# Kernel optimization log

Hardware: AMD Instinct MI355X
Metric: run time of the kernel (lower is better)

The kernel has to match this reference:

```python
import jax, jax.numpy as jnp
import numpy as np

IN, OUT, R = 512, 512, 4
H = (IN + OUT) * R + OUT  # 4608, LSTM hidden size


def setup_inputs() -> dict:
    key = jax.random.key(0)
    ks = jax.random.split(key, 8)
    B = 256
    x = jax.random.normal(ks[0], (B, IN), dtype=jnp.float32)
    h0 = jax.random.normal(ks[1], (B, H), dtype=jnp.float32)
    c0 = jax.random.normal(ks[2], (B, H), dtype=jnp.float32)
    s_ih = 1.0 / np.sqrt(H)
    W_ih = jax.random.uniform(ks[3], (4 * H, IN), dtype=jnp.float32, minval=-s_ih, maxval=s_ih)
    W_hh = jax.random.uniform(ks[4], (4 * H, H), dtype=jnp.float32, minval=-s_ih, maxval=s_ih)
    b_ih = jax.random.uniform(ks[5], (4 * H,), dtype=jnp.float32, minval=-s_ih, maxval=s_ih)
    b_hh = jax.random.uniform(ks[6], (4 * H,), dtype=jnp.float32, minval=-s_ih, maxval=s_ih)
    initial_weight = jax.random.normal(ks[7], (1, OUT, IN), dtype=jnp.float32)
    initial_bias = jnp.zeros((1, OUT), dtype=jnp.float32)
    return {"x": x, "h0": h0, "c0": c0, "W_ih": W_ih, "W_hh": W_hh,
            "b_ih": b_ih, "b_hh": b_hh,
            "initial_weight": initial_weight, "initial_bias": initial_bias}


def reference(x, h0, c0, W_ih, W_hh, b_ih, b_hh, initial_weight, initial_bias):
    B = x.shape[0]
    # Batched LSTMCell (the per-sample python loop in the original is
    # mathematically identical to one batched cell).  PyTorch gate order: i,f,g,o.
    gates = x @ W_ih.T + b_ih + h0 @ W_hh.T + b_hh  # [B, 4H]
    i, f, g, o = jnp.split(gates, 4, axis=-1)
    c_new = jax.nn.sigmoid(f) * c0 + jax.nn.sigmoid(i) * jnp.tanh(g)
    h_new = jax.nn.sigmoid(o) * jnp.tanh(c_new)  # [B, H]
    # Low-rank per-sample weight deltas
    dw1 = h_new[:, : OUT * R].reshape(B, OUT, R)
    dw2 = h_new[:, OUT * R: OUT * R + IN * R].reshape(B, R, IN)
    db = h_new[:, OUT * R + IN * R:]  # [B, OUT]
    weight = initial_weight + jnp.einsum('bor,bri->boi', dw1, dw2)  # [B, OUT, IN]
    bias = initial_bias + db  # [B, OUT]
    y = jnp.einsum('bi,boi->bo', x, weight) + bias
    return (y, h_new, c_new)
```

## Files before the change

### kernel.cpp

```cpp
#include <hip/hip_runtime.h>

#define B_DIM 256
#define H_DIM 4608
#define K_X   512
#define K_TOT 5120
#define NSTEP 160

typedef __attribute__((ext_vector_type(8))) short  short8;
typedef __attribute__((ext_vector_type(4))) float  floatx4;

#define BAR() do { \
  __builtin_amdgcn_sched_barrier(0); \
  asm volatile("s_waitcnt lgkmcnt(0)" ::: "memory"); \
  __builtin_amdgcn_s_barrier(); \
  __builtin_amdgcn_sched_barrier(0); \
} while (0)

static __device__ __forceinline__ unsigned pkbf(float a, float b){
  unsigned ua = (__float_as_uint(a) + 0x8000u) >> 16;
  unsigned ub = (__float_as_uint(b) + 0x8000u) & 0xFFFF0000u;
  return ua | ub;
}
static __device__ __forceinline__ float sigm(float v){ return 1.0f / (1.0f + __expf(-v)); }
static __device__ __forceinline__ float tanh_fast(float v){
  float ax = fabsf(v);
  float e  = __expf(-2.0f * ax);
  float t  = (1.0f - e) / (1.0f + e);
  return copysignf(t, v);
}

__global__ __launch_bounds__(256) void conv_kernel(
    const float* __restrict__ x, const float* __restrict__ h0,
    unsigned short* __restrict__ Abf, float* __restrict__ z)
{
  const int t = threadIdx.x;
  if (blockIdx.x == 0) ((float4*)z)[t] = make_float4(0.f, 0.f, 0.f, 0.f);
  const long e = ((long)blockIdx.x * 256 + t) * 8;
  const int  b = (int)(e / K_TOT);
  const int  k = (int)(e - (long)b * K_TOT);
  const float* src = (k < K_X) ? (x + (long)b * K_X + k)
                               : (h0 + (long)b * H_DIM + (k - K_X));
  float4 v0 = *(const float4*)src;
  float4 v1 = *(const float4*)(src + 4);
  uint4 wv;
  wv.x = pkbf(v0.x, v0.y); wv.y = pkbf(v0.z, v0.w);
  wv.z = pkbf(v1.x, v1.y); wv.w = pkbf(v1.z, v1.w);
  *(uint4*)(Abf + e) = wv;
}

__global__ __launch_bounds__(256, 2) void lstm_gates_kernel(
    const unsigned short* __restrict__ Abf,
    const float* __restrict__ x,
    const float* __restrict__ c0,
    const float* __restrict__ Wih, const float* __restrict__ Whh,
    const float* __restrict__ bih, const float* __restrict__ bhh,
    float* __restrict__ outH, float* __restrict__ outC,
    float* __restrict__ z)
{
  __shared__ __align__(16) unsigned short Bs[2][64 * 32];

  const int t    = threadIdx.x;
  const int j0   = blockIdx.x * 16;
  const int w    = t >> 6;
  const int l    = t & 63;
  const int q    = l >> 4;
  const int col  = l & 15;
  const int jj   = j0 + col;
  const int wrow = w * 64;

  const long aBase = (long)(wrow + col) * K_TOT + q * 8;

  const int  rB   = t >> 2;
  const int  cB   = t & 3;
  const int  gate = rB >> 4;
  const int  jl   = rB & 15;
  const long wrowg = (long)gate * H_DIM + j0 + jl;
  const float* __restrict__ pWx = Wih + wrowg * K_X   + cB * 8;
  const float* __restrict__ pWh = Whh + wrowg * H_DIM + cB * 8;

  char* ldsBase = (char*)&Bs[0][0];
  const int bwByte = rB  * 64 + ((cB ^ ((rB  >> 1) & 3)) << 4);
  const int brByte = col * 64 + ((q  ^ ((col >> 1) & 3)) << 4);

  floatx4 acc[4][4];
  #pragma unroll
  for (int nt = 0; nt < 4; ++nt){
    float bsum = bih[nt * H_DIM + jj] + bhh[nt * H_DIM + jj];
    floatx4 v = {bsum, bsum, bsum, bsum};
    #pragma unroll
    for (int mt = 0; mt < 4; ++mt) acc[mt][nt] = v;
  }

  float4 pb[4][2];
  short8 af0[4], af1[4];

  auto issueB = [&](int kt, int slot){
    const int ko = kt * 32;
    const float* p = (ko < K_X) ? (pWx + ko) : (pWh + (ko - K_X));
    pb[slot][0] = *(const float4*)p;
    pb[slot][1] = *(const float4*)(p + 4);
  };
  auto writeB = [&](int slot, int buf){
    uint4 wv;
    wv.x = pkbf(pb[slot][0].x, pb[slot][0].y);
    wv.y = pkbf(pb[slot][0].z, pb[slot][0].w);
    wv.z = pkbf(pb[slot][1].x, pb[slot][1].y);
    wv.w = pkbf(pb[slot][1].z, pb[slot][1].w);
    *(uint4*)(ldsBase + buf * 4096 + bwByte) = wv;
  };
  auto loadA = [&](int kt, short8* af){
    const unsigned short* p = Abf + (aBase + kt * 32);
    #pragma unroll
    for (int mt = 0; mt < 4; ++mt)
      af[mt] = *(const short8*)(p + (long)mt * (16 * K_TOT));
  };
  auto mfmaStep = [&](int buf, const short8* af){
    short8 bf[4];
    #pragma unroll
    for (int nt = 0; nt < 4; ++nt)
      bf[nt] = *(const short8*)(ldsBase + buf * 4096 + brByte + nt * 1024);
    #pragma unroll
    for (int mt = 0; mt < 4; ++mt)
      #pragma unroll
      for (int nt = 0; nt < 4; ++nt)
        acc[mt][nt] = __builtin_amdgcn_mfma_f32_16x16x32_bf16(af[mt], bf[nt], acc[mt][nt], 0, 0, 0);
  };

  issueB(0, 0); issueB(1, 1); issueB(2, 2); issueB(3, 3);
  loadA(0, af0);
  writeB(0, 0);
  BAR();

  #pragma unroll 1
  for (int k = 0; k < NSTEP; k += 4){
    loadA(k + 1, af1);
    if (k + 4 < NSTEP) issueB(k + 4, 0);
    mfmaStep(0, af0);
    writeB(1, 1);
    BAR();
    loadA(k + 2, af0);
    if (k + 5 < NSTEP) issueB(k + 5, 1);
    mfmaStep(1, af1);
    writeB(2, 0);
    BAR();
    loadA(k + 3, af1);
    if (k + 6 < NSTEP) issueB(k + 6, 2);
    mfmaStep(0, af0);
    writeB(3, 1);
    BAR();
    if (k + 4 < NSTEP) loadA(k + 4, af0);
    if (k + 7 < NSTEP) issueB(k + 7, 3);
    mfmaStep(1, af1);
    if (k + 4 < NSTEP) writeB(0, 0);
    BAR();
  }

  const bool isDw2 = (j0 >= 2048) && (j0 < 4096);
  const int  rIdx  = (j0 - 2048) >> 9;
  const int  i0    = (j0 - 2048) & 511;

  #pragma unroll
  for (int mt = 0; mt < 4; ++mt){
    #pragma unroll
    for (int r2 = 0; r2 < 4; ++r2){
      const int brow = wrow + mt * 16 + q * 4 + r2;
      float iv = acc[mt][0][r2];
      float fv = acc[mt][1][r2];
      float gv = acc[mt][2][r2];
      float ov = acc[mt][3][r2];
      float cp = c0[(long)brow * H_DIM + jj];
      float cn = sigm(fv) * cp + sigm(iv) * tanh_fast(gv);
      float hn = sigm(ov) * tanh_fast(cn);
      outH[(long)brow * H_DIM + jj] = hn;
      outC[(long)brow * H_DIM + jj] = cn;
      if (isDw2){
        float v = hn * x[(long)brow * K_X + i0 + col];
        v += __shfl_xor(v, 1); v += __shfl_xor(v, 2);
        v += __shfl_xor(v, 4); v += __shfl_xor(v, 8);
        if (col == 0) atomicAdd(&z[brow * 4 + rIdx], v);
      }
    }
  }
}

__global__ __launch_bounds__(256) void y_kernel(
    const unsigned short* __restrict__ Abf,
    const float* __restrict__ hnew,
    const float* __restrict__ W0, const float* __restrict__ b0,
    const float* __restrict__ z,
    float* __restrict__ y)
{
  __shared__ __align__(16) unsigned short Ws[16 * 512];
  const int t    = threadIdx.x;
  const int w    = t >> 6;
  const int l    = t & 63;
  const int q    = l >> 4;
  const int col  = l & 15;
  const int n0   = blockIdx.x * 16;
  const int wrow = w * 64;

  {
    const int r  = t >> 4;
    const int kc = (t & 15) * 32;
    const float* src = W0 + (long)(n0 + r) * 512 + kc;
    #pragma unroll
    for (int j = 0; j < 4; ++j){
      float4 a = *(const float4*)(src + j * 8);
      float4 b = *(const float4*)(src + j * 8 + 4);
      uint4 wv;
      wv.x = pkbf(a.x, a.y); wv.y = pkbf(a.z, a.w);
      wv.z = pkbf(b.x, b.y); wv.w = pkbf(b.z, b.w);
      const int cch = (kc >> 3) + j;
      const int sw  = cch ^ (r & 7);
      *(uint4*)((char*)Ws + r * 1024 + sw * 16) = wv;
    }
  }
  __syncthreads();

  const long aBase = (long)(wrow + col) * K_TOT + q * 8;
  floatx4 acc[4];
  #pragma unroll
  for (int mt = 0; mt < 4; ++mt) acc[mt] = (floatx4){0.f, 0.f, 0.f, 0.f};

  #pragma unroll 4
  for (int ks = 0; ks < 16; ++ks){
    const int sw = (ks * 4 + q) ^ (col & 7);
    short8 bf = *(const short8*)((char*)Ws + col * 1024 + sw * 16);
    #pragma unroll
    for (int mt = 0; mt < 4; ++mt){
      short8 af = *(const short8*)(Abf + aBase + ks * 32 + (long)mt * (16 * K_TOT));
      acc[mt] = __builtin_amdgcn_mfma_f32_16x16x32_bf16(af, bf, acc[mt], 0, 0, 0);
    }
  }

  const int   o  = n0 + col;
  const float bo = b0[o];
  #pragma unroll
  for (int mt = 0; mt < 4; ++mt){
    #pragma unroll
    for (int r2 = 0; r2 < 4; ++r2){
      const int brow = wrow + mt * 16 + q * 4 + r2;
      const float* hr = hnew + (long)brow * H_DIM;
      float4 d1 = *(const float4*)(hr + o * 4);
      float4 zr = *(const float4*)(z + brow * 4);
      float val = acc[mt][r2] + bo + hr[4096 + o]
                + d1.x * zr.x + d1.y * zr.y + d1.z * zr.z + d1.w * zr.w;
      y[(long)brow * 512 + o] = val;
    }
  }
}

extern "C" void kernel_launch(void* const* d_in, const int* in_sizes, int n_in,
                              void* d_out, int out_size, void* d_ws, size_t ws_size,
                              hipStream_t stream)
{
  (void)in_sizes; (void)n_in; (void)out_size; (void)ws_size;
  const float* x   = (const float*)d_in[0];
  const float* h0  = (const float*)d_in[1];
  const float* c0  = (const float*)d_in[2];
  const float* Wih = (const float*)d_in[3];
  const float* Whh = (const float*)d_in[4];
  const float* bih = (const float*)d_in[5];
  const float* bhh = (const float*)d_in[6];
  const float* W0  = (const float*)d_in[7];
  const float* b0  = (const float*)d_in[8];

  float* out  = (float*)d_out;
  float* y    = out;
  float* outH = out + 131072;
  float* outC = out + 131072 + 1179648;

  unsigned short* Abf = (unsigned short*)d_ws;
  float* z = (float*)((char*)d_ws + (size_t)B_DIM * K_TOT * 2);

  hipLaunchKernelGGL(conv_kernel, dim3(640), dim3(256), 0, stream, x, h0, Abf, z);
  hipLaunchKernelGGL(lstm_gates_kernel, dim3(288), dim3(256), 0, stream,
                     Abf, x, c0, Wih, Whh, bih, bhh, outH, outC, z);
  hipLaunchKernelGGL(y_kernel, dim3(32), dim3(256), 0, stream, Abf, outH, W0, b0, z, y);
}
```

Baseline: 677.5 us.

## Split-K the LSTM gate GEMM with atomic accumulation and a separate cell kernel

The gate GEMM is split four ways along K, so 1152 blocks run instead of 288, and the occupancy hint rises to 4 blocks per CU. This addresses the under-filled GPU: 288 blocks is barely more than one wave of blocks across the CUs. Partial sums go by float atomicAdd into a zeroed fp32 gate buffer, and a new cell_kernel then adds biases, applies the LSTM nonlinearity and computes the dw2 dot products. The cost is an extra kernel launch, zeroing and re-reading about 19 MB of gate scratch, and a large number of global atomics.

Result: slower. 860.4 us (+27.0%).

```diff
diff --git a/kernel.cpp b/kernel.cpp
--- a/kernel.cpp
+++ b/kernel.cpp
@@ -4,7 +4,10 @@
 #define H_DIM 4608
 #define K_X   512
 #define K_TOT 5120
-#define NSTEP 160
+#define NSPLIT 4
+#define KSPL  (K_TOT / NSPLIT)
+#define NSTEP (KSPL / 32)
+#define G_STRIDE 18432
 
 typedef __attribute__((ext_vector_type(8))) short  short8;
 typedef __attribute__((ext_vector_type(4))) float  floatx4;
@@ -31,10 +34,18 @@
 
 __global__ __launch_bounds__(256) void conv_kernel(
     const float* __restrict__ x, const float* __restrict__ h0,
-    unsigned short* __restrict__ Abf, float* __restrict__ z)
+    unsigned short* __restrict__ Abf, float* __restrict__ G,
+    float* __restrict__ z)
 {
   const int t = threadIdx.x;
   if (blockIdx.x == 0) ((float4*)z)[t] = make_float4(0.f, 0.f, 0.f, 0.f);
+
+  {
+    float4 z4 = make_float4(0.f, 0.f, 0.f, 0.f);
+    for (int i = blockIdx.x * 256 + t; i < 1179648; i += 640 * 256)
+      ((float4*)G)[i] = z4;
+  }
+
   const long e = ((long)blockIdx.x * 256 + t) * 8;
   const int  b = (int)(e / K_TOT);
   const int  k = (int)(e - (long)b * K_TOT);
@@ -48,27 +59,26 @@
   *(uint4*)(Abf + e) = wv;
 }
 
-__global__ __launch_bounds__(256, 2) void lstm_gates_kernel(
+__global__ __launch_bounds__(256, 4) void lstm_gates_kernel(
     const unsigned short* __restrict__ Abf,
-    const float* __restrict__ x,
-    const float* __restrict__ c0,
     const float* __restrict__ Wih, const float* __restrict__ Whh,
-    const float* __restrict__ bih, const float* __restrict__ bhh,
-    float* __restrict__ outH, float* __restrict__ outC,
-    float* __restrict__ z)
+    float* __restrict__ G)
 {
   __shared__ __align__(16) unsigned short Bs[2][64 * 32];
 
-  const int t    = threadIdx.x;
-  const int j0   = blockIdx.x * 16;
-  const int w    = t >> 6;
-  const int l    = t & 63;
-  const int q    = l >> 4;
-  const int col  = l & 15;
-  const int jj   = j0 + col;
-  const int wrow = w * 64;
-
-  const long aBase = (long)(wrow + col) * K_TOT + q * 8;
+  const int t     = threadIdx.x;
+  const int tile  = blockIdx.x >> 2;
+  const int split = blockIdx.x & 3;
+  const int kbase = split * KSPL;
+  const int j0    = tile * 16;
+  const int w     = t >> 6;
+  const int l     = t & 63;
+  const int q     = l >> 4;
+  const int col   = l & 15;
+  const int jj    = j0 + col;
+  const int wrow  = w * 64;
+
+  const long aBase = (long)(wrow + col) * K_TOT + kbase + q * 8;
 
   const int  rB   = t >> 2;
   const int  cB   = t & 3;
@@ -84,18 +94,16 @@
 
   floatx4 acc[4][4];
   #pragma unroll
-  for (int nt = 0; nt < 4; ++nt){
-    float bsum = bih[nt * H_DIM + jj] + bhh[nt * H_DIM + jj];
-    floatx4 v = {bsum, bsum, bsum, bsum};
-    #pragma unroll
-    for (int mt = 0; mt < 4; ++mt) acc[mt][nt] = v;
-  }
+  for (int mt = 0; mt < 4; ++mt)
+    #pragma unroll
+    for (int nt = 0; nt < 4; ++nt)
+      acc[mt][nt] = (floatx4){0.f, 0.f, 0.f, 0.f};
 
   float4 pb[4][2];
   short8 af0[4], af1[4];
 
   auto issueB = [&](int kt, int slot){
-    const int ko = kt * 32;
+    const int ko = kbase + kt * 32;
     const float* p = (ko < K_X) ? (pWx + ko) : (pWh + (ko - K_X));
     pb[slot][0] = *(const float4*)p;
     pb[slot][1] = *(const float4*)(p + 4);
@@ -155,30 +163,67 @@
     BAR();
   }
 
-  const bool isDw2 = (j0 >= 2048) && (j0 < 4096);
-  const int  rIdx  = (j0 - 2048) >> 9;
-  const int  i0    = (j0 - 2048) & 511;
-
   #pragma unroll
   for (int mt = 0; mt < 4; ++mt){
     #pragma unroll
     for (int r2 = 0; r2 < 4; ++r2){
       const int brow = wrow + mt * 16 + q * 4 + r2;
-      float iv = acc[mt][0][r2];
-      float fv = acc[mt][1][r2];
-      float gv = acc[mt][2][r2];
-      float ov = acc[mt][3][r2];
-      float cp = c0[(long)brow * H_DIM + jj];
-      float cn = sigm(fv) * cp + sigm(iv) * tanh_fast(gv);
-      float hn = sigm(ov) * tanh_fast(cn);
-      outH[(long)brow * H_DIM + jj] = hn;
-      outC[(long)brow * H_DIM + jj] = cn;
-      if (isDw2){
-        float v = hn * x[(long)brow * K_X + i0 + col];
-        v += __shfl_xor(v, 1); v += __shfl_xor(v, 2);
-        v += __shfl_xor(v, 4); v += __shfl_xor(v, 8);
-        if (col == 0) atomicAdd(&z[brow * 4 + rIdx], v);
-      }
+      float* gp = G + (long)brow * G_STRIDE + jj;
+      atomicAdd(gp,            acc[mt][0][r2]);
+      atomicAdd(gp + H_DIM,    acc[mt][1][r2]);
+      atomicAdd(gp + 2*H_DIM,  acc[mt][2][r2]);
+      atomicAdd(gp + 3*H_DIM,  acc[mt][3][r2]);
+    }
+  }
+}
+
+__global__ __launch_bounds__(256) void cell_kernel(
+    const float* __restrict__ G, const float* __restrict__ c0,
+    const float* __restrict__ bih, const float* __restrict__ bhh,
+    const float* __restrict__ x,
+    float* __restrict__ outH, float* __restrict__ outC, float* __restrict__ z)
+{
+  const int b = blockIdx.x;
+  const int t = threadIdx.x;
+  const int l = t & 63;
+
+  const float4* Gf  = (const float4*)(G  + (long)b * G_STRIDE);
+  const float4* cf  = (const float4*)(c0 + (long)b * H_DIM);
+  const float4* bi4 = (const float4*)bih;
+  const float4* bh4 = (const float4*)bhh;
+  const float4* x4  = (const float4*)(x + (long)b * K_X);
+  float4* H4 = (float4*)(outH + (long)b * H_DIM);
+  float4* C4 = (float4*)(outC + (long)b * H_DIM);
+
+  for (int v = t; v < 1152; v += 256){
+    float4 gi = Gf[v];
+    float4 gf = Gf[1152 + v];
+    float4 gg = Gf[2304 + v];
+    float4 go = Gf[3456 + v];
+    float4 b0i = bi4[v],        b0h = bh4[v];
+    float4 b1i = bi4[1152 + v], b1h = bh4[1152 + v];
+    float4 b2i = bi4[2304 + v], b2h = bh4[2304 + v];
+    float4 b3i = bi4[3456 + v], b3h = bh4[3456 + v];
+    gi.x += b0i.x + b0h.x; gi.y += b0i.y + b0h.y; gi.z += b0i.z + b0h.z; gi.w += b0i.w + b0h.w;
+    gf.x += b1i.x + b1h.x; gf.y += b1i.y + b1h.y; gf.z += b1i.z + b1h.z; gf.w += b1i.w + b1h.w;
+    gg.x += b2i.x + b2h.x; gg.y += b2i.y + b2h.y; gg.z += b2i.z + b2h.z; gg.w += b2i.w + b2h.w;
+    go.x += b3i.x + b3h.x; go.y += b3i.y + b3h.y; go.z += b3i.z + b3h.z; go.w += b3i.w + b3h.w;
+    float4 cp = cf[v];
+    float4 cn, hn;
+    cn.x = sigm(gf.x) * cp.x + sigm(gi.x) * tanh_fast(gg.x); hn.x = sigm(go.x) * tanh_fast(cn.x);
+    cn.y = sigm(gf.y) * cp.y + sigm(gi.y) * tanh_fast(gg.y); hn.y = sigm(go.y) * tanh_fast(cn.y);
+    cn.z = sigm(gf.z) * cp.z + sigm(gi.z) * tanh_fast(gg.z); hn.z = sigm(go.z) * tanh_fast(cn.z);
+    cn.w = sigm(gf.w) * cp.w + sigm(gi.w) * tanh_fast(gg.w); hn.w = sigm(go.w) * tanh_fast(cn.w);
+    C4[v] = cn;
+    H4[v] = hn;
+    const int j = v * 4;
+    if (j >= 2048 && j < 4096){
+      const int r = (j - 2048) >> 9;
+      float4 xv = x4[v - 512 - (r << 7)];
+      float s = hn.x * xv.x + hn.y * xv.y + hn.z * xv.z + hn.w * xv.w;
+      s += __shfl_xor(s, 32); s += __shfl_xor(s, 16); s += __shfl_xor(s, 8);
+      s += __shfl_xor(s, 4);  s += __shfl_xor(s, 2);  s += __shfl_xor(s, 1);
+      if (l == 0) atomicAdd(&z[b * 4 + r], s);
     }
   }
 }
@@ -272,9 +317,12 @@
 
   unsigned short* Abf = (unsigned short*)d_ws;
   float* z = (float*)((char*)d_ws + (size_t)B_DIM * K_TOT * 2);
-
-  hipLaunchKernelGGL(conv_kernel, dim3(640), dim3(256), 0, stream, x, h0, Abf, z);
-  hipLaunchKernelGGL(lstm_gates_kernel, dim3(288), dim3(256), 0, stream,
-                     Abf, x, c0, Wih, Whh, bih, bhh, outH, outC, z);
+  float* G = (float*)((char*)d_ws + (size_t)B_DIM * K_TOT * 2 + 4096);
+
+  hipLaunchKernelGGL(conv_kernel, dim3(640), dim3(256), 0, stream, x, h0, Abf, G, z);
+  hipLaunchKernelGGL(lstm_gates_kernel, dim3(288 * NSPLIT), dim3(256), 0, stream,
+                     Abf, Wih, Whh, G);
+  hipLaunchKernelGGL(cell_kernel, dim3(256), dim3(256), 0, stream,
+                     G, c0, bih, bhh, x, outH, outC, z);
   hipLaunchKernelGGL(y_kernel, dim3(32), dim3(256), 0, stream, Abf, outH, W0, b0, z, y);
 }
```

## Split fused LSTM GEMM into transposed LDS-free GEMM plus separate cell kernel

Applied to the files above, without the earlier changes.

Replaces the fused gates GEMM and cell kernel with two kernels. The first computes the transposed gate matrix, with weights as the A operand loaded straight from global memory and converted to bf16 in registers, over 1152 blocks with no LDS or barriers. The second applies the cell nonlinearity through LDS-staged tiles and writes coalesced h/c. This raises parallelism and removes barrier stalls, at the cost of a 19 MB fp32 gate intermediate round-trip through memory and an extra launch.

After: 986.4 us. 45.6% more time.

```diff
diff --git a/kernel.cpp b/kernel.cpp
--- a/kernel.cpp
+++ b/kernel.cpp
@@ -4,17 +4,10 @@
 #define H_DIM 4608
 #define K_X   512
 #define K_TOT 5120
-#define NSTEP 160
-
-typedef __attribute__((ext_vector_type(8))) short  short8;
-typedef __attribute__((ext_vector_type(4))) float  floatx4;
-
-#define BAR() do { \
-  __builtin_amdgcn_sched_barrier(0); \
-  asm volatile("s_waitcnt lgkmcnt(0)" ::: "memory"); \
-  __builtin_amdgcn_s_barrier(); \
-  __builtin_amdgcn_sched_barrier(0); \
-} while (0)
+
+typedef __attribute__((ext_vector_type(8))) short    short8;
+typedef __attribute__((ext_vector_type(4))) float    floatx4;
+typedef __attribute__((ext_vector_type(4))) unsigned uintx4;
 
 static __device__ __forceinline__ unsigned pkbf(float a, float b){
   unsigned ua = (__float_as_uint(a) + 0x8000u) >> 16;
@@ -35,6 +28,7 @@
 {
   const int t = threadIdx.x;
   if (blockIdx.x == 0) ((float4*)z)[t] = make_float4(0.f, 0.f, 0.f, 0.f);
+
   const long e = ((long)blockIdx.x * 256 + t) * 8;
   const int  b = (int)(e / K_TOT);
   const int  k = (int)(e - (long)b * K_TOT);
@@ -48,137 +42,117 @@
   *(uint4*)(Abf + e) = wv;
 }
 
-__global__ __launch_bounds__(256, 2) void lstm_gates_kernel(
+__global__ __launch_bounds__(256, 4) void gatesT_kernel(
     const unsigned short* __restrict__ Abf,
+    const float* __restrict__ Wih, const float* __restrict__ Whh,
+    float* __restrict__ GT)
+{
+  const int t   = threadIdx.x;
+  const int w   = t >> 6;
+  const int l   = t & 63;
+  const int q   = l >> 4;
+  const int col = l & 15;
+  const int m0  = blockIdx.x * 16;
+  const int wb  = w * 64;
+
+  const float* __restrict__ pWx = Wih + (long)(m0 + col) * K_X   + q * 8;
+  const float* __restrict__ pWh = Whh + (long)(m0 + col) * H_DIM + q * 8;
+  const unsigned short* __restrict__ pA0 = Abf + (long)(wb + col) * K_TOT + q * 8;
+  const unsigned short* __restrict__ pA1 = pA0 + (long)16 * K_TOT;
+  const unsigned short* __restrict__ pA2 = pA0 + (long)32 * K_TOT;
+  const unsigned short* __restrict__ pA3 = pA0 + (long)48 * K_TOT;
+
+  floatx4 acc0 = {0.f,0.f,0.f,0.f}, acc1 = acc0, acc2 = acc0, acc3 = acc0;
+
+#define GSTEP(PW, AOFF) do {                                                   \
+    floatx4 w0 = *(const floatx4*)(PW);                                        \
+    floatx4 w1 = *(const floatx4*)((PW) + 4);                                  \
+    union { uintx4 u; short8 s; } cv;                                          \
+    cv.u = (uintx4){ pkbf(w0.x,w0.y), pkbf(w0.z,w0.w),                         \
+                     pkbf(w1.x,w1.y), pkbf(w1.z,w1.w) };                       \
+    short8 af = cv.s;                                                          \
+    acc0 = __builtin_amdgcn_mfma_f32_16x16x32_bf16(af, *(const short8*)(pA0 + (AOFF)), acc0, 0, 0, 0); \
+    acc1 = __builtin_amdgcn_mfma_f32_16x16x32_bf16(af, *(const short8*)(pA1 + (AOFF)), acc1, 0, 0, 0); \
+    acc2 = __builtin_amdgcn_mfma_f32_16x16x32_bf16(af, *(const short8*)(pA2 + (AOFF)), acc2, 0, 0, 0); \
+    acc3 = __builtin_amdgcn_mfma_f32_16x16x32_bf16(af, *(const short8*)(pA3 + (AOFF)), acc3, 0, 0, 0); \
+  } while (0)
+
+  #pragma unroll 4
+  for (int kt = 0; kt < 16; ++kt)
+    GSTEP(pWx + kt * 32, kt * 32);
+  #pragma unroll 4
+  for (int kt = 0; kt < 144; ++kt)
+    GSTEP(pWh + kt * 32, K_X + kt * 32);
+#undef GSTEP
+
+  float* __restrict__ gp = GT + (long)(m0 + q * 4) * B_DIM + wb + col;
+  #pragma unroll
+  for (int r = 0; r < 4; ++r){
+    gp[(long)r * B_DIM +  0] = acc0[r];
+    gp[(long)r * B_DIM + 16] = acc1[r];
+    gp[(long)r * B_DIM + 32] = acc2[r];
+    gp[(long)r * B_DIM + 48] = acc3[r];
+  }
+}
+
+__global__ __launch_bounds__(256) void cell_kernel(
+    const float* __restrict__ GT, const float* __restrict__ c0,
+    const float* __restrict__ bih, const float* __restrict__ bhh,
     const float* __restrict__ x,
-    const float* __restrict__ c0,
-    const float* __restrict__ Wih, const float* __restrict__ Whh,
-    const float* __restrict__ bih, const float* __restrict__ bhh,
-    float* __restrict__ outH, float* __restrict__ outC,
-    float* __restrict__ z)
-{
-  __shared__ __align__(16) unsigned short Bs[2][64 * 32];
-
-  const int t    = threadIdx.x;
-  const int j0   = blockIdx.x * 16;
-  const int w    = t >> 6;
-  const int l    = t & 63;
-  const int q    = l >> 4;
-  const int col  = l & 15;
-  const int jj   = j0 + col;
-  const int wrow = w * 64;
-
-  const long aBase = (long)(wrow + col) * K_TOT + q * 8;
-
-  const int  rB   = t >> 2;
-  const int  cB   = t & 3;
-  const int  gate = rB >> 4;
-  const int  jl   = rB & 15;
-  const long wrowg = (long)gate * H_DIM + j0 + jl;
-  const float* __restrict__ pWx = Wih + wrowg * K_X   + cB * 8;
-  const float* __restrict__ pWh = Whh + wrowg * H_DIM + cB * 8;
-
-  char* ldsBase = (char*)&Bs[0][0];
-  const int bwByte = rB  * 64 + ((cB ^ ((rB  >> 1) & 3)) << 4);
-  const int brByte = col * 64 + ((q  ^ ((col >> 1) & 3)) << 4);
-
-  floatx4 acc[4][4];
-  #pragma unroll
-  for (int nt = 0; nt < 4; ++nt){
-    float bsum = bih[nt * H_DIM + jj] + bhh[nt * H_DIM + jj];
-    floatx4 v = {bsum, bsum, bsum, bsum};
-    #pragma unroll
-    for (int mt = 0; mt < 4; ++mt) acc[mt][nt] = v;
-  }
-
-  float4 pb[4][2];
-  short8 af0[4], af1[4];
-
-  auto issueB = [&](int kt, int slot){
-    const int ko = kt * 32;
-    const float* p = (ko < K_X) ? (pWx + ko) : (pWh + (ko - K_X));
-    pb[slot][0] = *(const float4*)p;
-    pb[slot][1] = *(const float4*)(p + 4);
-  };
-  auto writeB = [&](int slot, int buf){
-    uint4 wv;
-    wv.x = pkbf(pb[slot][0].x, pb[slot][0].y);
-    wv.y = pkbf(pb[slot][0].z, pb[slot][0].w);
-    wv.z = pkbf(pb[slot][1].x, pb[slot][1].y);
-    wv.w = pkbf(pb[slot][1].z, pb[slot][1].w);
-    *(uint4*)(ldsBase + buf * 4096 + bwByte) = wv;
-  };
-  auto loadA = [&](int kt, short8* af){
-    const unsigned short* p = Abf + (aBase + kt * 32);
-    #pragma unroll
-    for (int mt = 0; mt < 4; ++mt)
-      af[mt] = *(const short8*)(p + (long)mt * (16 * K_TOT));
-  };
-  auto mfmaStep = [&](int buf, const short8* af){
-    short8 bf[4];
-    #pragma unroll
-    for (int nt = 0; nt < 4; ++nt)
-      bf[nt] = *(const short8*)(ldsBase + buf * 4096 + brByte + nt * 1024);
-    #pragma unroll
-    for (int mt = 0; mt < 4; ++mt)
-      #pragma unroll
-      for (int nt = 0; nt < 4; ++nt)
-        acc[mt][nt] = __builtin_amdgcn_mfma_f32_16x16x32_bf16(af[mt], bf[nt], acc[mt][nt], 0, 0, 0);
-  };
-
-  issueB(0, 0); issueB(1, 1); issueB(2, 2); issueB(3, 3);
-  loadA(0, af0);
-  writeB(0, 0);
-  BAR();
-
-  #pragma unroll 1
-  for (int k = 0; k < NSTEP; k += 4){
-    loadA(k + 1, af1);
-    if (k + 4 < NSTEP) issueB(k + 4, 0);
-    mfmaStep(0, af0);
-    writeB(1, 1);
-    BAR();
-    loadA(k + 2, af0);
-    if (k + 5 < NSTEP) issueB(k + 5, 1);
-    mfmaStep(1, af1);
-    writeB(2, 0);
-    BAR();
-    loadA(k + 3, af1);
-    if (k + 6 < NSTEP) issueB(k + 6, 2);
-    mfmaStep(0, af0);
-    writeB(3, 1);
-    BAR();
-    if (k + 4 < NSTEP) loadA(k + 4, af0);
-    if (k + 7 < NSTEP) issueB(k + 7, 3);
-    mfmaStep(1, af1);
-    if (k + 4 < NSTEP) writeB(0, 0);
-    BAR();
-  }
-
+    float* __restrict__ outH, float* __restrict__ outC, float* __restrict__ z)
+{
+  __shared__ float cs[128][67];
+  __shared__ float hs[128][67];
+  __shared__ float xs[128][67];
+
+  const int t  = threadIdx.x;
+  const int j0 = (blockIdx.x >> 1) * 64;
+  const int bh = blockIdx.x & 1;
   const bool isDw2 = (j0 >= 2048) && (j0 < 4096);
-  const int  rIdx  = (j0 - 2048) >> 9;
-  const int  i0    = (j0 - 2048) & 511;
-
-  #pragma unroll
-  for (int mt = 0; mt < 4; ++mt){
-    #pragma unroll
-    for (int r2 = 0; r2 < 4; ++r2){
-      const int brow = wrow + mt * 16 + q * 4 + r2;
-      float iv = acc[mt][0][r2];
-      float fv = acc[mt][1][r2];
-      float gv = acc[mt][2][r2];
-      float ov = acc[mt][3][r2];
-      float cp = c0[(long)brow * H_DIM + jj];
-      float cn = sigm(fv) * cp + sigm(iv) * tanh_fast(gv);
-      float hn = sigm(ov) * tanh_fast(cn);
-      outH[(long)brow * H_DIM + jj] = hn;
-      outC[(long)brow * H_DIM + jj] = cn;
-      if (isDw2){
-        float v = hn * x[(long)brow * K_X + i0 + col];
-        v += __shfl_xor(v, 1); v += __shfl_xor(v, 2);
-        v += __shfl_xor(v, 4); v += __shfl_xor(v, 8);
-        if (col == 0) atomicAdd(&z[brow * 4 + rIdx], v);
-      }
+  const int rIdx = (j0 - 2048) >> 9;
+  const int i0   = (j0 - 2048) & 511;
+
+  {
+    const int jj = t & 63;
+    const int bb = t >> 6;
+    for (int p = 0; p < 32; ++p){
+      const int b = p * 4 + bb;
+      cs[b][jj] = c0[(long)(bh * 128 + b) * H_DIM + j0 + jj];
+      if (isDw2) xs[b][jj] = x[(long)(bh * 128 + b) * K_X + i0 + jj];
+    }
+  }
+  __syncthreads();
+
+  {
+    const int b  = t & 127;
+    const int jh = t >> 7;
+    float zacc = 0.f;
+    for (int jj = 0; jj < 32; ++jj){
+      const int j  = jh * 32 + jj;
+      const int jg = j0 + j;
+      const long cbase = (long)jg * B_DIM + bh * 128 + b;
+      float gi = GT[cbase]                            + bih[jg]             + bhh[jg];
+      float gf = GT[cbase + (long)H_DIM * B_DIM]      + bih[H_DIM + jg]     + bhh[H_DIM + jg];
+      float gg = GT[cbase + (long)2 * H_DIM * B_DIM]  + bih[2 * H_DIM + jg] + bhh[2 * H_DIM + jg];
+      float go = GT[cbase + (long)3 * H_DIM * B_DIM]  + bih[3 * H_DIM + jg] + bhh[3 * H_DIM + jg];
+      float cp = cs[b][j];
+      float cn = sigm(gf) * cp + sigm(gi) * tanh_fast(gg);
+      float hn = sigm(go) * tanh_fast(cn);
+      cs[b][j] = cn;
+      hs[b][j] = hn;
+      if (isDw2) zacc += hn * xs[b][j];
+    }
+    if (isDw2) atomicAdd(&z[(bh * 128 + b) * 4 + rIdx], zacc);
+  }
+  __syncthreads();
+
+  {
+    const int jj = t & 63;
+    const int bb = t >> 6;
+    for (int p = 0; p < 32; ++p){
+      const int b = p * 4 + bb;
+      outC[(long)(bh * 128 + b) * H_DIM + j0 + jj] = cs[b][jj];
+      outH[(long)(bh * 128 + b) * H_DIM + j0 + jj] = hs[b][jj];
     }
   }
 }
@@ -271,10 +245,13 @@
   float* outC = out + 131072 + 1179648;
 
   unsigned short* Abf = (unsigned short*)d_ws;
-  float* z = (float*)((char*)d_ws + (size_t)B_DIM * K_TOT * 2);
+  float* z  = (float*)((char*)d_ws + (size_t)B_DIM * K_TOT * 2);
+  float* GT = (float*)((char*)d_ws + (size_t)B_DIM * K_TOT * 2 + 4096);
 
   hipLaunchKernelGGL(conv_kernel, dim3(640), dim3(256), 0, stream, x, h0, Abf, z);
-  hipLaunchKernelGGL(lstm_gates_kernel, dim3(288), dim3(256), 0, stream,
-                     Abf, x, c0, Wih, Whh, bih, bhh, outH, outC, z);
+  hipLaunchKernelGGL(gatesT_kernel, dim3(1152), dim3(256), 0, stream,
+                     Abf, Wih, Whh, GT);
+  hipLaunchKernelGGL(cell_kernel, dim3(144), dim3(256), 0, stream,
+                     GT, c0, bih, bhh, x, outH, outC, z);
   hipLaunchKernelGGL(y_kernel, dim3(32), dim3(256), 0, stream, Abf, outH, W0, b0, z, y);
 }
```
